# Kernel tuning notes

Measured on AMD Instinct MI355X. Metric: run time of the kernel, lower is better.

Reference implementation:

```python
import jax, jax.numpy as jnp
import numpy as np

N_NODES = 100000
N_EDGES = 1600000
D_IN = 128
D_OUT = 128


def setup_inputs() -> dict:
    key = jax.random.key(0)
    k1, k2, k3, k4, k5 = jax.random.split(key, 5)
    H = jax.random.normal(k1, (N_NODES, D_IN), dtype=jnp.float32)
    vals = jax.random.uniform(k2, (N_EDGES,), dtype=jnp.float32)
    W = jax.random.normal(k3, (D_OUT, D_IN), dtype=jnp.float32) * (1.0 / np.sqrt(D_IN))
    rows = jax.random.randint(k4, (N_EDGES,), 0, N_NODES, dtype=jnp.int32)
    cols = jax.random.randint(k5, (N_EDGES,), 0, N_NODES, dtype=jnp.int32)
    return {"H": H, "vals": vals, "W": W, "rows": rows, "cols": cols}


def reference(H, vals, W, rows, cols):
    # Single-rank: communicate_fgm is a no-op (X is zeros, no remote peers).
    # SpMM: out[i] = sum_e vals[e] * H[cols[e]] for edges with rows[e] == i
    msgs = vals[:, None] * H[cols]                      # [n_edges, d_in] irregular gather
    AH = jax.ops.segment_sum(msgs, rows, num_segments=N_NODES)  # [n_nodes, d_in]
    # Linear (no bias) + ReLU
    out = jax.nn.relu(AH @ W.T)                          # [n_nodes, d_out]
    return out
```

## Files before the change

kernel.cpp:

```cpp
#include <hip/hip_runtime.h>

#define N_NODES 100000
#define N_EDGES 1600000
#define D 128

#define NB 782
#define SLOT 2560
#define CHUNK 6400
#define NBLK_BUCKET 250

#define WB_OFF     0u
#define HWB_OFF    65536u
#define BCNT_OFF   25665536u
#define RANGES_OFF 25669632u
#define EPACK0_OFF 26472448u
#define EPACK1_OFF 42487808u

typedef unsigned int uint;
typedef __attribute__((ext_vector_type(4))) float f32x4;
typedef __attribute__((ext_vector_type(8))) short bf16x8;

__device__ __forceinline__ unsigned short f2bf(float x) {
    uint u = __float_as_uint(x);
    uint r = u + 0x7fffu + ((u >> 16) & 1u);
    return (unsigned short)(r >> 16);
}

__global__ void k_cast_w(const float* __restrict__ W, unsigned short* __restrict__ Wb) {
    int i = blockIdx.x * blockDim.x + threadIdx.x;
    Wb[i] = f2bf(W[i]);
}

__global__ __launch_bounds__(256) void k_gemm_mfma(const float* __restrict__ H,
                                                   const unsigned short* __restrict__ Wb,
                                                   unsigned short* __restrict__ HWb) {
    const int wave = threadIdx.x >> 6;
    const int lane = threadIdx.x & 63;
    const int rowtile = blockIdx.x * 4 + wave;
    if (rowtile >= N_NODES / 16) return;
    const int rowbase = rowtile * 16;
    const int m    = lane & 15;
    const int quad = lane >> 4;

    f32x4 acc[8];
    #pragma unroll
    for (int nt = 0; nt < 8; ++nt) acc[nt] = (f32x4){0.f, 0.f, 0.f, 0.f};

    const float* hrow = H + (size_t)(rowbase + m) * D;

    #pragma unroll
    for (int ks = 0; ks < 4; ++ks) {
        const int k0 = ks * 32 + quad * 8;
        float4 a0 = *(const float4*)(hrow + k0);
        float4 a1 = *(const float4*)(hrow + k0 + 4);
        bf16x8 afr;
        afr[0] = (short)f2bf(a0.x); afr[1] = (short)f2bf(a0.y);
        afr[2] = (short)f2bf(a0.z); afr[3] = (short)f2bf(a0.w);
        afr[4] = (short)f2bf(a1.x); afr[5] = (short)f2bf(a1.y);
        afr[6] = (short)f2bf(a1.z); afr[7] = (short)f2bf(a1.w);
        #pragma unroll
        for (int nt = 0; nt < 8; ++nt) {
            bf16x8 bfr = *(const bf16x8*)(Wb + (size_t)(nt * 16 + m) * D + k0);
            acc[nt] = __builtin_amdgcn_mfma_f32_16x16x32_bf16(afr, bfr, acc[nt], 0, 0, 0);
        }
    }

    #pragma unroll
    for (int nt = 0; nt < 8; ++nt) {
        #pragma unroll
        for (int r = 0; r < 4; ++r) {
            int orow = rowbase + quad * 4 + r;
            HWb[(size_t)orow * D + nt * 16 + m] = f2bf(acc[nt][r]);
        }
    }
}

__global__ __launch_bounds__(256) void k_bucket_coarse(const int* __restrict__ rows,
                                                       const int* __restrict__ cols,
                                                       const float* __restrict__ vals,
                                                       int* __restrict__ bcnt,
                                                       int2* __restrict__ epack0) {
    __shared__ int srows[CHUNK];
    __shared__ int hist[NB];
    __shared__ int cur[NB];
    const int tid = threadIdx.x;
    const int e0  = blockIdx.x * CHUNK;

    for (int b = tid; b < NB; b += 256) hist[b] = 0;
    __syncthreads();

    for (int i = tid; i < CHUNK; i += 256) {
        int r = rows[e0 + i];
        srows[i] = r;
        atomicAdd(&hist[r >> 7], 1);
    }
    __syncthreads();

    for (int b = tid; b < NB; b += 256) {
        int c = hist[b];
        int base = (c > 0) ? atomicAdd(&bcnt[b], c) : 0;
        cur[b] = b * SLOT + base;
    }
    __syncthreads();

    for (int i = tid; i < CHUNK; i += 256) {
        int r = srows[i];
        int b = r >> 7;
        int p = atomicAdd(&cur[b], 1);
        epack0[p] = make_int2(((r & 127) << 17) | cols[e0 + i],
                              __float_as_int(vals[e0 + i]));
    }
}

__global__ __launch_bounds__(256) void k_sort_bucket(const int* __restrict__ bcnt,
                                                     const int2* __restrict__ epack0,
                                                     int2* __restrict__ epack1,
                                                     int2* __restrict__ ranges) {
    __shared__ int2 se[SLOT];
    __shared__ int hist[128];
    __shared__ int sc[128];
    __shared__ int cur[128];
    const int tid  = threadIdx.x;
    const int b    = blockIdx.x;
    const int base = b * SLOT;
    const int n_e  = bcnt[b];

    if (tid < 128) hist[tid] = 0;
    __syncthreads();

    for (int i = tid; i < n_e; i += 256) {
        int2 e = epack0[base + i];
        se[i] = e;
        atomicAdd(&hist[e.x >> 17], 1);
    }
    __syncthreads();

    if (tid < 128) sc[tid] = hist[tid];
    __syncthreads();
    #pragma unroll
    for (int off = 1; off < 128; off <<= 1) {
        int t = (tid < 128 && tid >= off) ? sc[tid - off] : 0;
        __syncthreads();
        if (tid < 128) sc[tid] += t;
        __syncthreads();
    }
    if (tid < 128) {
        int ex = sc[tid] - hist[tid];
        cur[tid] = ex;
        int row = b * 128 + tid;
        if (row < N_NODES)
            ranges[row] = make_int2(base + ex, base + ex + hist[tid]);
    }
    __syncthreads();

    for (int i = tid; i < n_e; i += 256) {
        int2 e  = se[i];
        int  lr = e.x >> 17;
        int  p  = atomicAdd(&cur[lr], 1);
        epack1[base + p] = make_int2(e.x & 0x1FFFF, e.y);
    }
}

__global__ __launch_bounds__(256) void k_spmm_gather(const unsigned short* __restrict__ HWb,
                                                     const int2* __restrict__ ranges,
                                                     const int2* __restrict__ epack,
                                                     float* __restrict__ out) {
    int gid  = blockIdx.x * blockDim.x + threadIdx.x;
    int node = gid >> 4;
    int lane = gid & 15;
    if (node >= N_NODES) return;
    int2 rg = ranges[node];

    float acc[8];
    #pragma unroll
    for (int c = 0; c < 8; ++c) acc[c] = 0.f;

    for (int j = rg.x; j < rg.y; ++j) {
        int2  e = epack[j];
        float v = __int_as_float(e.y);
        uint4 q = ((const uint4*)(HWb + (size_t)e.x * D))[lane];
        acc[0] = fmaf(v, __uint_as_float(q.x << 16),         acc[0]);
        acc[1] = fmaf(v, __uint_as_float(q.x & 0xffff0000u), acc[1]);
        acc[2] = fmaf(v, __uint_as_float(q.y << 16),         acc[2]);
        acc[3] = fmaf(v, __uint_as_float(q.y & 0xffff0000u), acc[3]);
        acc[4] = fmaf(v, __uint_as_float(q.z << 16),         acc[4]);
        acc[5] = fmaf(v, __uint_as_float(q.z & 0xffff0000u), acc[5]);
        acc[6] = fmaf(v, __uint_as_float(q.w << 16),         acc[6]);
        acc[7] = fmaf(v, __uint_as_float(q.w & 0xffff0000u), acc[7]);
    }

    float4 o0 = make_float4(fmaxf(acc[0], 0.f), fmaxf(acc[1], 0.f),
                            fmaxf(acc[2], 0.f), fmaxf(acc[3], 0.f));
    float4 o1 = make_float4(fmaxf(acc[4], 0.f), fmaxf(acc[5], 0.f),
                            fmaxf(acc[6], 0.f), fmaxf(acc[7], 0.f));
    ((float4*)out)[node * 32 + lane * 2]     = o0;
    ((float4*)out)[node * 32 + lane * 2 + 1] = o1;
}

extern "C" void kernel_launch(void* const* d_in, const int* in_sizes, int n_in,
                              void* d_out, int out_size, void* d_ws, size_t ws_size,
                              hipStream_t stream) {
    const float* H    = (const float*)d_in[0];
    const float* vals = (const float*)d_in[1];
    const float* W    = (const float*)d_in[2];
    const int*   rows = (const int*)d_in[3];
    const int*   cols = (const int*)d_in[4];
    float* out = (float*)d_out;

    char* ws = (char*)d_ws;
    unsigned short* Wb     = (unsigned short*)(ws + WB_OFF);
    unsigned short* HWb    = (unsigned short*)(ws + HWB_OFF);
    int*            bcnt   = (int*)(ws + BCNT_OFF);
    int2*           ranges = (int2*)(ws + RANGES_OFF);
    int2*           epack0 = (int2*)(ws + EPACK0_OFF);
    int2*           epack1 = (int2*)(ws + EPACK1_OFF);

    k_cast_w<<<64, 256, 0, stream>>>(W, Wb);
    k_gemm_mfma<<<(N_NODES / 16 + 3) / 4, 256, 0, stream>>>(H, Wb, HWb);

    hipMemsetAsync(bcnt, 0, NB * sizeof(int), stream);
    k_bucket_coarse<<<NBLK_BUCKET, 256, 0, stream>>>(rows, cols, vals, bcnt, epack0);
    k_sort_bucket<<<NB, 256, 0, stream>>>(bcnt, epack0, epack1, ranges);

    k_spmm_gather<<<(N_NODES * 16 + 255) / 256, 256, 0, stream>>>(HWb, ranges, epack1, out);
}
```

Before: 282.0 us.

## Fuse per-bucket sort with SpMM gather using shared-memory edge lists

Merges the bucket sort kernel and the SpMM gather kernel into one kernel. Each block sorts its bucket's edges by local row into LDS and then gathers HW rows directly, so the epack1 and ranges arrays no longer round-trip through global memory. The gather loop is unrolled by four to keep more loads in flight. The cost is that each block now handles 128 rows with only 16 row-groups, giving 782 blocks of 256 threads. That means less parallelism in the gather phase and LDS use of about 20KB per block, which could reduce latency hiding.

```diff
diff --git a/kernel.cpp b/kernel.cpp
--- a/kernel.cpp
+++ b/kernel.cpp
@@ -12,9 +12,7 @@
 #define WB_OFF     0u
 #define HWB_OFF    65536u
 #define BCNT_OFF   25665536u
-#define RANGES_OFF 25669632u
-#define EPACK0_OFF 26472448u
-#define EPACK1_OFF 42487808u
+#define EPACK0_OFF 25669632u
 
 typedef unsigned int uint;
 typedef __attribute__((ext_vector_type(4))) float f32x4;
@@ -24,6 +22,17 @@
     uint u = __float_as_uint(x);
     uint r = u + 0x7fffu + ((u >> 16) & 1u);
     return (unsigned short)(r >> 16);
+}
+
+__device__ __forceinline__ void acc8(float acc[8], uint4 q, float v) {
+    acc[0] = fmaf(v, __uint_as_float(q.x << 16),         acc[0]);
+    acc[1] = fmaf(v, __uint_as_float(q.x & 0xffff0000u), acc[1]);
+    acc[2] = fmaf(v, __uint_as_float(q.y << 16),         acc[2]);
+    acc[3] = fmaf(v, __uint_as_float(q.y & 0xffff0000u), acc[3]);
+    acc[4] = fmaf(v, __uint_as_float(q.z << 16),         acc[4]);
+    acc[5] = fmaf(v, __uint_as_float(q.z & 0xffff0000u), acc[5]);
+    acc[6] = fmaf(v, __uint_as_float(q.w << 16),         acc[6]);
+    acc[7] = fmaf(v, __uint_as_float(q.w & 0xffff0000u), acc[7]);
 }
 
 __global__ void k_cast_w(const float* __restrict__ W, unsigned short* __restrict__ Wb) {
@@ -112,14 +121,16 @@
     }
 }
 
-__global__ __launch_bounds__(256) void k_sort_bucket(const int* __restrict__ bcnt,
-                                                     const int2* __restrict__ epack0,
-                                                     int2* __restrict__ epack1,
-                                                     int2* __restrict__ ranges) {
-    __shared__ int2 se[SLOT];
+__global__ __launch_bounds__(256) void k_spmm_fused(const int* __restrict__ bcnt,
+                                                    const int2* __restrict__ epack0,
+                                                    const unsigned short* __restrict__ HWb,
+                                                    float* __restrict__ out) {
+    __shared__ int   scol[SLOT];
+    __shared__ float sval[SLOT];
     __shared__ int hist[128];
     __shared__ int sc[128];
     __shared__ int cur[128];
+    __shared__ int rstart[128];
     const int tid  = threadIdx.x;
     const int b    = blockIdx.x;
     const int base = b * SLOT;
@@ -128,11 +139,8 @@
     if (tid < 128) hist[tid] = 0;
     __syncthreads();
 
-    for (int i = tid; i < n_e; i += 256) {
-        int2 e = epack0[base + i];
-        se[i] = e;
-        atomicAdd(&hist[e.x >> 17], 1);
-    }
+    for (int i = tid; i < n_e; i += 256)
+        atomicAdd(&hist[epack0[base + i].x >> 17], 1);
     __syncthreads();
 
     if (tid < 128) sc[tid] = hist[tid];
@@ -146,55 +154,60 @@
     }
     if (tid < 128) {
         int ex = sc[tid] - hist[tid];
+        rstart[tid] = ex;
         cur[tid] = ex;
-        int row = b * 128 + tid;
-        if (row < N_NODES)
-            ranges[row] = make_int2(base + ex, base + ex + hist[tid]);
     }
     __syncthreads();
 
     for (int i = tid; i < n_e; i += 256) {
-        int2 e  = se[i];
+        int2 e  = epack0[base + i];
         int  lr = e.x >> 17;
         int  p  = atomicAdd(&cur[lr], 1);
-        epack1[base + p] = make_int2(e.x & 0x1FFFF, e.y);
-    }
-}
-
-__global__ __launch_bounds__(256) void k_spmm_gather(const unsigned short* __restrict__ HWb,
-                                                     const int2* __restrict__ ranges,
-                                                     const int2* __restrict__ epack,
-                                                     float* __restrict__ out) {
-    int gid  = blockIdx.x * blockDim.x + threadIdx.x;
-    int node = gid >> 4;
-    int lane = gid & 15;
-    if (node >= N_NODES) return;
-    int2 rg = ranges[node];
-
-    float acc[8];
-    #pragma unroll
-    for (int c = 0; c < 8; ++c) acc[c] = 0.f;
-
-    for (int j = rg.x; j < rg.y; ++j) {
-        int2  e = epack[j];
-        float v = __int_as_float(e.y);
-        uint4 q = ((const uint4*)(HWb + (size_t)e.x * D))[lane];
-        acc[0] = fmaf(v, __uint_as_float(q.x << 16),         acc[0]);
-        acc[1] = fmaf(v, __uint_as_float(q.x & 0xffff0000u), acc[1]);
-        acc[2] = fmaf(v, __uint_as_float(q.y << 16),         acc[2]);
-        acc[3] = fmaf(v, __uint_as_float(q.y & 0xffff0000u), acc[3]);
-        acc[4] = fmaf(v, __uint_as_float(q.z << 16),         acc[4]);
-        acc[5] = fmaf(v, __uint_as_float(q.z & 0xffff0000u), acc[5]);
-        acc[6] = fmaf(v, __uint_as_float(q.w << 16),         acc[6]);
-        acc[7] = fmaf(v, __uint_as_float(q.w & 0xffff0000u), acc[7]);
-    }
-
-    float4 o0 = make_float4(fmaxf(acc[0], 0.f), fmaxf(acc[1], 0.f),
-                            fmaxf(acc[2], 0.f), fmaxf(acc[3], 0.f));
-    float4 o1 = make_float4(fmaxf(acc[4], 0.f), fmaxf(acc[5], 0.f),
-                            fmaxf(acc[6], 0.f), fmaxf(acc[7], 0.f));
-    ((float4*)out)[node * 32 + lane * 2]     = o0;
-    ((float4*)out)[node * 32 + lane * 2 + 1] = o1;
+        scol[p] = e.x & 0x1FFFF;
+        sval[p] = __int_as_float(e.y);
+    }
+    __syncthreads();
+
+    const int lane  = tid & 15;
+    const int group = tid >> 4;
+
+    #pragma unroll
+    for (int rr = 0; rr < 8; ++rr) {
+        const int lr  = group * 8 + rr;
+        const int row = b * 128 + lr;
+        if (row >= N_NODES) continue;
+        const int s  = rstart[lr];
+        const int e_ = cur[lr];
+
+        float acc[8];
+        #pragma unroll
+        for (int c = 0; c < 8; ++c) acc[c] = 0.f;
+
+        int j = s;
+        for (; j + 3 < e_; j += 4) {
+            int   c0 = scol[j],     c1 = scol[j + 1], c2 = scol[j + 2], c3 = scol[j + 3];
+            float v0 = sval[j],     v1 = sval[j + 1], v2 = sval[j + 2], v3 = sval[j + 3];
+            uint4 q0 = ((const uint4*)(HWb + (size_t)c0 * D))[lane];
+            uint4 q1 = ((const uint4*)(HWb + (size_t)c1 * D))[lane];
+            uint4 q2 = ((const uint4*)(HWb + (size_t)c2 * D))[lane];
+            uint4 q3 = ((const uint4*)(HWb + (size_t)c3 * D))[lane];
+            acc8(acc, q0, v0); acc8(acc, q1, v1);
+            acc8(acc, q2, v2); acc8(acc, q3, v3);
+        }
+        for (; j < e_; ++j) {
+            int   c = scol[j];
+            float v = sval[j];
+            uint4 q = ((const uint4*)(HWb + (size_t)c * D))[lane];
+            acc8(acc, q, v);
+        }
+
+        float4 o0 = make_float4(fmaxf(acc[0], 0.f), fmaxf(acc[1], 0.f),
+                                fmaxf(acc[2], 0.f), fmaxf(acc[3], 0.f));
+        float4 o1 = make_float4(fmaxf(acc[4], 0.f), fmaxf(acc[5], 0.f),
+                                fmaxf(acc[6], 0.f), fmaxf(acc[7], 0.f));
+        ((float4*)out)[row * 32 + lane * 2]     = o0;
+        ((float4*)out)[row * 32 + lane * 2 + 1] = o1;
+    }
 }
 
 extern "C" void kernel_launch(void* const* d_in, const int* in_sizes, int n_in,
@@ -211,16 +224,12 @@
     unsigned short* Wb     = (unsigned short*)(ws + WB_OFF);
     unsigned short* HWb    = (unsigned short*)(ws + HWB_OFF);
     int*            bcnt   = (int*)(ws + BCNT_OFF);
-    int2*           ranges = (int2*)(ws + RANGES_OFF);
     int2*           epack0 = (int2*)(ws + EPACK0_OFF);
-    int2*           epack1 = (int2*)(ws + EPACK1_OFF);
 
     k_cast_w<<<64, 256, 0, stream>>>(W, Wb);
     k_gemm_mfma<<<(N_NODES / 16 + 3) / 4, 256, 0, stream>>>(H, Wb, HWb);
 
     hipMemsetAsync(bcnt, 0, NB * sizeof(int), stream);
     k_bucket_coarse<<<NBLK_BUCKET, 256, 0, stream>>>(rows, cols, vals, bcnt, epack0);
-    k_sort_bucket<<<NB, 256, 0, stream>>>(bcnt, epack0, epack1, ranges);
-
-    k_spmm_gather<<<(N_NODES * 16 + 255) / 256, 256, 0, stream>>>(HWb, ranges, epack1, out);
-}
+    k_spmm_fused<<<NB, 256, 0, stream>>>(bcnt, epack0, HWb, out);
+}
```

New measurement: 264.4 us. 6.2% less time.
